# Kernel optimization log

Measured on AMD Instinct MI355X. Metric: run time of the kernel, lower is better.

Reference implementation:

```python
import jax, jax.numpy as jnp
import numpy as np

B, S, DIM, H = 2, 4096, 512, 8
HD = DIM // H
SCALE = HD ** -0.5
EPS = 1e-5


def setup_inputs() -> dict:
    key = jax.random.key(0)
    ks = jax.random.split(key, 7)
    std = DIM ** -0.5
    return {
        "x": jax.random.normal(ks[0], (B, S, DIM), dtype=jnp.float32),
        "ln_gamma": jnp.ones((DIM,), jnp.float32),
        "ln_beta": jnp.zeros((DIM,), jnp.float32),
        "w_q": jax.random.normal(ks[1], (DIM, DIM), jnp.float32) * std,
        "w_k": jax.random.normal(ks[2], (DIM, DIM), jnp.float32) * std,
        "w_v": jax.random.normal(ks[3], (DIM, DIM), jnp.float32) * std,
        "w_fc": jax.random.normal(ks[4], (DIM, DIM), jnp.float32) * std,
    }


def reference(x, ln_gamma, ln_beta, w_q, w_k, w_v, w_fc):
    # LayerNorm over last dim
    mu = jnp.mean(x, axis=-1, keepdims=True)
    var = jnp.var(x, axis=-1, keepdims=True)
    xn = (x - mu) * jax.lax.rsqrt(var + EPS) * ln_gamma + ln_beta
    # QKV projections (torch Linear: y = x @ W.T), split into heads -> [B,H,S,HD]
    q = jnp.einsum('bsd,ed->bse', xn, w_q).reshape(B, S, H, HD).transpose(0, 2, 1, 3)
    k = jnp.einsum('bsd,ed->bse', xn, w_k).reshape(B, S, H, HD).transpose(0, 2, 1, 3)
    v = jnp.einsum('bsd,ed->bse', xn, w_v).reshape(B, S, H, HD).transpose(0, 2, 1, 3)
    # scores [B,H,S,S]
    attn = jnp.einsum('bhqd,bhkd->bhqk', q, k) * SCALE
    attn = jax.nn.softmax(attn, axis=-1)
    # dropout is identity in eval mode
    out = jnp.einsum('bhqk,bhkd->bhqd', attn, v)
    out = out.transpose(0, 2, 1, 3).reshape(B, S, DIM)
    return jnp.einsum('bsd,ed->bse', out, w_fc)
```

## Files before the change

kernel.cpp:

```cpp
#include <hip/hip_runtime.h>
#include <cstdint>
#include <cstddef>

typedef unsigned short u16;
typedef unsigned int   u32;
typedef __bf16 bf16x8 __attribute__((ext_vector_type(8)));
typedef float  f32x4  __attribute__((ext_vector_type(4)));
typedef float  f32x16 __attribute__((ext_vector_type(16)));
typedef u16    u16x8  __attribute__((ext_vector_type(8)));
typedef u16    u16x4  __attribute__((ext_vector_type(4)));
typedef u32    u32x2  __attribute__((ext_vector_type(2)));
typedef u32    u32x4  __attribute__((ext_vector_type(4)));

#define DI __device__ __forceinline__

constexpr int SEQ = 4096;
constexpr int DIM = 512;
constexpr int NH  = 8;
constexpr int HD  = 64;
constexpr float ATT_C1 = 0.125f * 1.44269504088896340736f;

DI u16 f2bf(float f) {
  u32 u = __builtin_bit_cast(u32, f);
  u += 0x7fffu + ((u >> 16) & 1u);
  return (u16)(u >> 16);
}

DI u32 pk2(float hi, float lo) {
  u32 uh = __builtin_bit_cast(u32, hi) + 0x8000u;
  u32 ul = __builtin_bit_cast(u32, lo) + 0x8000u;
  return __builtin_amdgcn_perm(uh, ul, 0x07060302u);
}

DI u32 cvtpk(float a, float b) {
  u32 r;
  asm("v_cvt_pk_bf16_f32 %0, %1, %2" : "=v"(r) : "v"(a), "v"(b));
  return r;
}

DI void plswap(u32& a, u32& b) {
  asm("v_permlane32_swap_b32 %0, %1" : "+v"(a), "+v"(b));
}

__global__ __launch_bounds__(256) void wconv_kernel(
    const float* __restrict__ wq, const float* __restrict__ wk,
    const float* __restrict__ wv, const float* __restrict__ wfc,
    u16* __restrict__ Wb)
{
  const int idx  = blockIdx.x * 256 + threadIdx.x;
  const int base = idx * 8;
  const int mat  = base >> 18;
  const int off  = base & (512 * 512 - 1);
  const float* src = (mat == 0) ? wq : (mat == 1) ? wk : (mat == 2) ? wv : wfc;
  const float4 a = *(const float4*)(src + off);
  const float4 b = *(const float4*)(src + off + 4);
  u32x4 o = { pk2(a.y, a.x), pk2(a.w, a.z), pk2(b.y, b.x), pk2(b.w, b.z) };
  *(u32x4*)(Wb + base) = o;
}

__global__ __launch_bounds__(256) void ln_cast_kernel(
    const float* __restrict__ x, const float* __restrict__ gamma,
    const float* __restrict__ beta, u16* __restrict__ xn)
{
  const int row  = blockIdx.x * 4 + (threadIdx.x >> 6);
  const int lane = threadIdx.x & 63;
  const float* xr = x + (size_t)row * DIM + lane * 8;
  const float4 a = *(const float4*)xr;
  const float4 b = *(const float4*)(xr + 4);
  float s = a.x + a.y + a.z + a.w + b.x + b.y + b.z + b.w;
  float q = a.x*a.x + a.y*a.y + a.z*a.z + a.w*a.w
          + b.x*b.x + b.y*b.y + b.z*b.z + b.w*b.w;
#pragma unroll
  for (int m = 1; m < 64; m <<= 1) {
    s += __shfl_xor(s, m, 64);
    q += __shfl_xor(q, m, 64);
  }
  const float mu = s * (1.0f / DIM);
  const float rs = rsqrtf(q * (1.0f / DIM) - mu * mu + 1e-5f);
  const float4 g0 = *(const float4*)(gamma + lane * 8);
  const float4 g1 = *(const float4*)(gamma + lane * 8 + 4);
  const float4 e0 = *(const float4*)(beta + lane * 8);
  const float4 e1 = *(const float4*)(beta + lane * 8 + 4);
  const float v0 = (a.x - mu) * rs * g0.x + e0.x;
  const float v1 = (a.y - mu) * rs * g0.y + e0.y;
  const float v2 = (a.z - mu) * rs * g0.z + e0.z;
  const float v3 = (a.w - mu) * rs * g0.w + e0.w;
  const float v4 = (b.x - mu) * rs * g1.x + e1.x;
  const float v5 = (b.y - mu) * rs * g1.y + e1.y;
  const float v6 = (b.z - mu) * rs * g1.z + e1.z;
  const float v7 = (b.w - mu) * rs * g1.w + e1.w;
  u32x4 o = { pk2(v1, v0), pk2(v3, v2), pk2(v5, v4), pk2(v7, v6) };
  *(u32x4*)(xn + (size_t)row * DIM + lane * 8) = o;
}

template<int MODE>
__global__ __launch_bounds__(256, 2) void gemm_kernel(
    const u16* __restrict__ A, const u16* __restrict__ Wb,
    u16* __restrict__ Qo, u16* __restrict__ Ko, u16* __restrict__ Vt,
    float* __restrict__ Co)
{
  __shared__ u16 As[128][72];
  __shared__ u16 Bs[128][72];
  const int m0 = blockIdx.y * 128, n0 = blockIdx.x * 128;
  const int t = threadIdx.x, wave = t >> 6, lane = t & 63;
  const int quad = lane >> 4, l15 = lane & 15;
  const int wm = wave >> 1, wn = wave & 1;
  const u16* Wsrc;
  if (MODE == 0) {
    const int mat = n0 >> 9;
    Wsrc = Wb + (size_t)mat * 512 * 512 + (size_t)(n0 & 511) * DIM;
  } else {
    Wsrc = Wb + (size_t)3 * 512 * 512 + (size_t)n0 * DIM;
  }

  f32x4 acc[4][4];
#pragma unroll
  for (int i = 0; i < 4; i++)
#pragma unroll
    for (int j = 0; j < 4; j++)
#pragma unroll
      for (int r = 0; r < 4; r++) acc[i][j][r] = 0.0f;

  for (int kk = 0; kk < DIM; kk += 64) {
    __syncthreads();
#pragma unroll
    for (int it = 0; it < 4; it++) {
      const int c4 = t + it * 256;
      const int r = c4 >> 3, off = (c4 & 7) * 8;
      *(u16x8*)&As[r][off] =
          *(const u16x8*)(A + (size_t)(m0 + r) * DIM + kk + off);
      *(u16x8*)&Bs[r][off] =
          *(const u16x8*)(Wsrc + (size_t)r * DIM + kk + off);
    }
    __syncthreads();
#pragma unroll
    for (int kx = 0; kx < 2; kx++) {
      bf16x8 af[4], bfr[4];
#pragma unroll
      for (int i = 0; i < 4; i++)
        af[i] = *(const bf16x8*)&As[wm * 64 + i * 16 + l15][kx * 32 + quad * 8];
#pragma unroll
      for (int j = 0; j < 4; j++)
        bfr[j] = *(const bf16x8*)&Bs[wn * 64 + j * 16 + l15][kx * 32 + quad * 8];
#pragma unroll
      for (int i = 0; i < 4; i++)
#pragma unroll
        for (int j = 0; j < 4; j++)
          acc[i][j] = __builtin_amdgcn_mfma_f32_16x16x32_bf16(
              af[i], bfr[j], acc[i][j], 0, 0, 0);
    }
  }

  if (MODE == 1) {
#pragma unroll
    for (int i = 0; i < 4; i++) {
      const int m = m0 + wm * 64 + i * 16 + quad * 4;
#pragma unroll
      for (int j = 0; j < 4; j++) {
        const int n = n0 + wn * 64 + j * 16 + l15;
#pragma unroll
        for (int r = 0; r < 4; r++)
          Co[(size_t)(m + r) * DIM + n] = acc[i][j][r];
      }
    }
  } else {
    const int mat = n0 >> 9;
    const float qs = (mat == 0) ? ATT_C1 : 1.0f;
#pragma unroll
    for (int i = 0; i < 4; i++) {
      const int m = m0 + wm * 64 + i * 16 + quad * 4;
      const int b = m >> 12, s = m & 4095;
#pragma unroll
      for (int j = 0; j < 4; j++) {
        const int ng = (n0 & 511) + wn * 64 + j * 16 + l15;
        const int h = ng >> 6, d = ng & 63;
        if (mat < 2) {
          u16* dst = (mat == 0 ? Qo : Ko) +
                     ((size_t)(b * NH + h) * SEQ) * HD + d;
#pragma unroll
          for (int r = 0; r < 4; r++)
            dst[(size_t)(s + r) * HD] = f2bf(acc[i][j][r] * qs);
        } else {
          u32x2 w;
          w[0] = pk2(acc[i][j][1], acc[i][j][0]);
          w[1] = pk2(acc[i][j][3], acc[i][j][2]);
          *(u32x2*)&Vt[((size_t)(b * NH + h) * HD + d) * SEQ + s] = w;
        }
      }
    }
  }
}

__global__ __launch_bounds__(256, 2) void attn_kernel(
    const u16* __restrict__ Q, const u16* __restrict__ K,
    const u16* __restrict__ Vt, u16* __restrict__ O)
{
  __shared__ __align__(16) char smem[36864];
  const int flat = blockIdx.x + 32 * blockIdx.y;
  const int slot = flat >> 3;
  const int bh = (flat & 7) * 2 + (slot & 1);
  const int qt = slot >> 1;
  const int b = bh >> 3, h = bh & 7;
  const int t = threadIdx.x;
  const int wave = t >> 6, lane = t & 63;
  const int kg = wave >> 1;
  const int qsub = wave & 1;
  const int tg = t & 127;
  const int l31 = lane & 31, hf = lane >> 5;

  u16 (*Kl)[72] = (u16 (*)[72])(smem + kg * 18432);
  u16 (*Vl)[72] = (u16 (*)[72])(smem + kg * 18432 + 9216);

  const u16* Qb = Q + (size_t)bh * SEQ * HD;
  const u16* Kb = K + (size_t)bh * SEQ * HD;
  const u16* Vb = Vt + (size_t)bh * HD * SEQ;
  const int qw = qt * 128 + qsub * 64;
  const int kc0 = kg * 2048;

  bf16x8 bq[2][4];
#pragma unroll
  for (int qh = 0; qh < 2; qh++)
#pragma unroll
    for (int kk = 0; kk < 4; kk++)
      bq[qh][kk] = *(const bf16x8*)(
          Qb + (size_t)(qw + qh * 32 + l31) * HD + kk * 16 + hf * 8);

  f32x16 oacc[2][2];
#pragma unroll
  for (int qh = 0; qh < 2; qh++)
#pragma unroll
    for (int mt2 = 0; mt2 < 2; mt2++)
#pragma unroll
      for (int r = 0; r < 16; r++) oacc[qh][mt2][r] = 0.0f;
  float lrun0 = 0.0f, lrun1 = 0.0f;

  u16x8 kst[4], vst[4];
#pragma unroll
  for (int it = 0; it < 4; it++) {
    const int c4 = tg + it * 128;
    const int r = c4 >> 3, off = (c4 & 7) * 8;
    kst[it] = *(const u16x8*)(Kb + (size_t)(kc0 + r) * HD + off);
    vst[it] = *(const u16x8*)(Vb + (size_t)r * SEQ + kc0 + off);
  }

  for (int it2 = 0; it2 < 32; it2++) {
    const int kc = kc0 + it2 * 64;
    __syncthreads();
#pragma unroll
    for (int it = 0; it < 4; it++) {
      const int c4 = tg + it * 128;
      const int r = c4 >> 3, off = (c4 & 7) * 8;
      *(u16x8*)&Kl[r][off] = kst[it];
      *(u16x8*)&Vl[r][off] = vst[it];
    }
    __syncthreads();
    if (it2 < 31) {
#pragma unroll
      for (int it = 0; it < 4; it++) {
        const int c4 = tg + it * 128;
        const int r = c4 >> 3, off = (c4 & 7) * 8;
        kst[it] = *(const u16x8*)(Kb + (size_t)(kc + 64 + r) * HD + off);
        vst[it] = *(const u16x8*)(Vb + (size_t)r * SEQ + kc + 64 + off);
      }
    }

#pragma unroll
    for (int mt = 0; mt < 2; mt++) {
      f32x16 s0, s1;
#pragma unroll
      for (int r = 0; r < 16; r++) { s0[r] = 0.0f; s1[r] = 0.0f; }
      __builtin_amdgcn_s_setprio(1);
#pragma unroll
      for (int kk = 0; kk < 4; kk++) {
        const bf16x8 ka =
            *(const bf16x8*)&Kl[mt * 32 + l31][kk * 16 + hf * 8];
        s0 = __builtin_amdgcn_mfma_f32_32x32x16_bf16(ka, bq[0][kk], s0, 0, 0, 0);
        s1 = __builtin_amdgcn_mfma_f32_32x32x16_bf16(ka, bq[1][kk], s1, 0, 0, 0);
      }
      __builtin_amdgcn_s_setprio(0);

#pragma unroll
      for (int r = 0; r < 16; r++) s0[r] = __builtin_amdgcn_exp2f(s0[r]);
      lrun0 += (((s0[0] + s0[1]) + (s0[2] + s0[3])) +
                ((s0[4] + s0[5]) + (s0[6] + s0[7]))) +
               (((s0[8] + s0[9]) + (s0[10] + s0[11])) +
                ((s0[12] + s0[13]) + (s0[14] + s0[15])));
#pragma unroll
      for (int r = 0; r < 16; r++) s1[r] = __builtin_amdgcn_exp2f(s1[r]);
      lrun1 += (((s1[0] + s1[1]) + (s1[2] + s1[3])) +
                ((s1[4] + s1[5]) + (s1[6] + s1[7]))) +
               (((s1[8] + s1[9]) + (s1[10] + s1[11])) +
                ((s1[12] + s1[13]) + (s1[14] + s1[15])));

      u32 a0 = cvtpk(s0[0],  s0[1]),  a1 = cvtpk(s0[2],  s0[3]);
      u32 a2 = cvtpk(s0[4],  s0[5]),  a3 = cvtpk(s0[6],  s0[7]);
      plswap(a0, a2); plswap(a1, a3);
      u32 c0 = cvtpk(s0[8],  s0[9]),  c1 = cvtpk(s0[10], s0[11]);
      u32 c2 = cvtpk(s0[12], s0[13]), c3 = cvtpk(s0[14], s0[15]);
      plswap(c0, c2); plswap(c1, c3);
      u32x4 p00v = { a0, a1, a2, a3 };
      u32x4 p01v = { c0, c1, c2, c3 };
      u32 d0 = cvtpk(s1[0],  s1[1]),  d1 = cvtpk(s1[2],  s1[3]);
      u32 d2 = cvtpk(s1[4],  s1[5]),  d3 = cvtpk(s1[6],  s1[7]);
      plswap(d0, d2); plswap(d1, d3);
      u32 e0 = cvtpk(s1[8],  s1[9]),  e1 = cvtpk(s1[10], s1[11]);
      u32 e2 = cvtpk(s1[12], s1[13]), e3 = cvtpk(s1[14], s1[15]);
      plswap(e0, e2); plswap(e1, e3);
      u32x4 p10v = { d0, d1, d2, d3 };
      u32x4 p11v = { e0, e1, e2, e3 };
      const bf16x8 p00 = __builtin_bit_cast(bf16x8, p00v);
      const bf16x8 p01 = __builtin_bit_cast(bf16x8, p01v);
      const bf16x8 p10 = __builtin_bit_cast(bf16x8, p10v);
      const bf16x8 p11 = __builtin_bit_cast(bf16x8, p11v);

      __builtin_amdgcn_s_setprio(1);
#pragma unroll
      for (int mt2 = 0; mt2 < 2; mt2++) {
        const bf16x8 va0 =
            *(const bf16x8*)&Vl[mt2 * 32 + l31][(mt * 2 + 0) * 16 + hf * 8];
        oacc[0][mt2] = __builtin_amdgcn_mfma_f32_32x32x16_bf16(
            va0, p00, oacc[0][mt2], 0, 0, 0);
        oacc[1][mt2] = __builtin_amdgcn_mfma_f32_32x32x16_bf16(
            va0, p10, oacc[1][mt2], 0, 0, 0);
        const bf16x8 va1 =
            *(const bf16x8*)&Vl[mt2 * 32 + l31][(mt * 2 + 1) * 16 + hf * 8];
        oacc[0][mt2] = __builtin_amdgcn_mfma_f32_32x32x16_bf16(
            va1, p01, oacc[0][mt2], 0, 0, 0);
        oacc[1][mt2] = __builtin_amdgcn_mfma_f32_32x32x16_bf16(
            va1, p11, oacc[1][mt2], 0, 0, 0);
      }
      __builtin_amdgcn_s_setprio(0);
    }
  }

  __syncthreads();
  f32x4 (*Rbuf)[2][8][64] = (f32x4 (*)[2][8][64])smem;
  float (*Lbuf)[2][64]    = (float (*)[2][64])(smem + 32768);
  if (kg == 1) {
#pragma unroll
    for (int qh = 0; qh < 2; qh++) {
#pragma unroll
      for (int mt2 = 0; mt2 < 2; mt2++)
#pragma unroll
        for (int gi = 0; gi < 4; gi++) {
          f32x4 w;
#pragma unroll
          for (int r = 0; r < 4; r++) w[r] = oacc[qh][mt2][gi * 4 + r];
          Rbuf[qsub][qh][mt2 * 4 + gi][lane] = w;
        }
      Lbuf[qsub][qh][lane] = (qh == 0) ? lrun0 : lrun1;
    }
  }
  __syncthreads();
  if (kg == 0) {
#pragma unroll
    for (int qh = 0; qh < 2; qh++) {
#pragma unroll
      for (int mt2 = 0; mt2 < 2; mt2++)
#pragma unroll
        for (int gi = 0; gi < 4; gi++) {
          const f32x4 w = Rbuf[qsub][qh][mt2 * 4 + gi][lane];
#pragma unroll
          for (int r = 0; r < 4; r++) oacc[qh][mt2][gi * 4 + r] += w[r];
        }
      float lr = ((qh == 0) ? lrun0 : lrun1) + Lbuf[qsub][qh][lane];
      const float lt = lr + __shfl_xor(lr, 32, 64);
      const float inv = 1.0f / lt;
      const int s = qw + qh * 32 + l31;
      u16* Ob = O + ((size_t)(b * SEQ + s)) * DIM + h * HD;
#pragma unroll
      for (int mt2 = 0; mt2 < 2; mt2++)
#pragma unroll
        for (int g = 0; g < 4; g++) {
          u32x2 w;
          w[0] = pk2(oacc[qh][mt2][g * 4 + 1] * inv,
                     oacc[qh][mt2][g * 4 + 0] * inv);
          w[1] = pk2(oacc[qh][mt2][g * 4 + 3] * inv,
                     oacc[qh][mt2][g * 4 + 2] * inv);
          *(u32x2*)&Ob[mt2 * 32 + g * 8 + hf * 4] = w;
        }
    }
  }
}

extern "C" void kernel_launch(void* const* d_in, const int* in_sizes, int n_in,
                              void* d_out, int out_size, void* d_ws,
                              size_t ws_size, hipStream_t stream)
{
  const float* x     = (const float*)d_in[0];
  const float* gamma = (const float*)d_in[1];
  const float* beta  = (const float*)d_in[2];
  const float* wq    = (const float*)d_in[3];
  const float* wk    = (const float*)d_in[4];
  const float* wv    = (const float*)d_in[5];
  const float* wfc   = (const float*)d_in[6];
  float* out = (float*)d_out;

  char* ws = (char*)d_ws;
  u16* xn = (u16*)(ws);
  u16* Qb = (u16*)(ws + ((size_t)8  << 20));
  u16* Kb = (u16*)(ws + ((size_t)16 << 20));
  u16* Vt = (u16*)(ws + ((size_t)24 << 20));
  u16* Ob = (u16*)(ws + ((size_t)32 << 20));
  u16* Wb = (u16*)(ws + ((size_t)40 << 20));

  wconv_kernel<<<512, 256, 0, stream>>>(wq, wk, wv, wfc, Wb);
  ln_cast_kernel<<<2048, 256, 0, stream>>>(x, gamma, beta, xn);
  gemm_kernel<0><<<dim3(12, 64), 256, 0, stream>>>(xn, Wb, Qb, Kb, Vt, nullptr);
  attn_kernel<<<dim3(32, 16), 256, 0, stream>>>(Qb, Kb, Vt, Ob);
  gemm_kernel<1><<<dim3(4, 64), 256, 0, stream>>>(
      Ob, Wb, nullptr, nullptr, nullptr, out);
}
```

Before: 196.7 us.

## Double-buffer attention K/V LDS tiles and use direct global-to-LDS loads in GEMM

The attention loop now keeps two K/V LDS buffers per key group. The next tile is written into the alternate buffer after compute, so each iteration needs one barrier instead of two. The GEMM staging switches to global_load_lds direct copies into unpadded LDS tiles, which skips the register round trip. In exchange, attention LDS use doubles to 72KB, which may cut occupancy, and the unpadded GEMM layout may add LDS bank conflicts on fragment reads.

```diff
diff --git a/kernel.cpp b/kernel.cpp
--- a/kernel.cpp
+++ b/kernel.cpp
@@ -40,6 +40,12 @@
 
 DI void plswap(u32& a, u32& b) {
   asm("v_permlane32_swap_b32 %0, %1" : "+v"(a), "+v"(b));
+}
+
+DI void gl_lds16(const void* g, void* lds) {
+  __builtin_amdgcn_global_load_lds(
+      (const __attribute__((address_space(1))) void*)g,
+      (__attribute__((address_space(3))) void*)lds, 16, 0, 0);
 }
 
 __global__ __launch_bounds__(256) void wconv_kernel(
@@ -99,8 +105,8 @@
     u16* __restrict__ Qo, u16* __restrict__ Ko, u16* __restrict__ Vt,
     float* __restrict__ Co)
 {
-  __shared__ u16 As[128][72];
-  __shared__ u16 Bs[128][72];
+  __shared__ __align__(16) u16 As[128 * 64];
+  __shared__ __align__(16) u16 Bs[128 * 64];
   const int m0 = blockIdx.y * 128, n0 = blockIdx.x * 128;
   const int t = threadIdx.x, wave = t >> 6, lane = t & 63;
   const int quad = lane >> 4, l15 = lane & 15;
@@ -124,13 +130,12 @@
   for (int kk = 0; kk < DIM; kk += 64) {
     __syncthreads();
 #pragma unroll
-    for (int it = 0; it < 4; it++) {
-      const int c4 = t + it * 256;
-      const int r = c4 >> 3, off = (c4 & 7) * 8;
-      *(u16x8*)&As[r][off] =
-          *(const u16x8*)(A + (size_t)(m0 + r) * DIM + kk + off);
-      *(u16x8*)&Bs[r][off] =
-          *(const u16x8*)(Wsrc + (size_t)r * DIM + kk + off);
+    for (int rnd = 0; rnd < 4; rnd++) {
+      const int c4 = t + rnd * 256;
+      const int r = c4 >> 3, cc = (c4 & 7) * 8;
+      const int lbase = (wave + rnd * 4) * 1024;
+      gl_lds16(A + (size_t)(m0 + r) * DIM + kk + cc, (char*)As + lbase);
+      gl_lds16(Wsrc + (size_t)r * DIM + kk + cc, (char*)Bs + lbase);
     }
     __syncthreads();
 #pragma unroll
@@ -138,10 +143,12 @@
       bf16x8 af[4], bfr[4];
 #pragma unroll
       for (int i = 0; i < 4; i++)
-        af[i] = *(const bf16x8*)&As[wm * 64 + i * 16 + l15][kx * 32 + quad * 8];
+        af[i] = *(const bf16x8*)&As[(wm * 64 + i * 16 + l15) * 64 +
+                                    kx * 32 + quad * 8];
 #pragma unroll
       for (int j = 0; j < 4; j++)
-        bfr[j] = *(const bf16x8*)&Bs[wn * 64 + j * 16 + l15][kx * 32 + quad * 8];
+        bfr[j] = *(const bf16x8*)&Bs[(wn * 64 + j * 16 + l15) * 64 +
+                                     kx * 32 + quad * 8];
 #pragma unroll
       for (int i = 0; i < 4; i++)
 #pragma unroll
@@ -195,7 +202,7 @@
     const u16* __restrict__ Q, const u16* __restrict__ K,
     const u16* __restrict__ Vt, u16* __restrict__ O)
 {
-  __shared__ __align__(16) char smem[36864];
+  __shared__ __align__(16) char smem[73728];
   const int flat = blockIdx.x + 32 * blockIdx.y;
   const int slot = flat >> 3;
   const int bh = (flat & 7) * 2 + (slot & 1);
@@ -208,9 +215,6 @@
   const int tg = t & 127;
   const int l31 = lane & 31, hf = lane >> 5;
 
-  u16 (*Kl)[72] = (u16 (*)[72])(smem + kg * 18432);
-  u16 (*Vl)[72] = (u16 (*)[72])(smem + kg * 18432 + 9216);
-
   const u16* Qb = Q + (size_t)bh * SEQ * HD;
   const u16* Kb = K + (size_t)bh * SEQ * HD;
   const u16* Vb = Vt + (size_t)bh * HD * SEQ;
@@ -242,27 +246,30 @@
     kst[it] = *(const u16x8*)(Kb + (size_t)(kc0 + r) * HD + off);
     vst[it] = *(const u16x8*)(Vb + (size_t)r * SEQ + kc0 + off);
   }
-
-  for (int it2 = 0; it2 < 32; it2++) {
-    const int kc = kc0 + it2 * 64;
-    __syncthreads();
+  {
+    u16 (*K0)[72] = (u16 (*)[72])(smem + kg * 36864);
+    u16 (*V0)[72] = (u16 (*)[72])(smem + kg * 36864 + 9216);
 #pragma unroll
     for (int it = 0; it < 4; it++) {
       const int c4 = tg + it * 128;
       const int r = c4 >> 3, off = (c4 & 7) * 8;
-      *(u16x8*)&Kl[r][off] = kst[it];
-      *(u16x8*)&Vl[r][off] = vst[it];
-    }
-    __syncthreads();
-    if (it2 < 31) {
-#pragma unroll
-      for (int it = 0; it < 4; it++) {
-        const int c4 = tg + it * 128;
-        const int r = c4 >> 3, off = (c4 & 7) * 8;
-        kst[it] = *(const u16x8*)(Kb + (size_t)(kc + 64 + r) * HD + off);
-        vst[it] = *(const u16x8*)(Vb + (size_t)r * SEQ + kc + 64 + off);
-      }
-    }
+      *(u16x8*)&K0[r][off] = kst[it];
+      *(u16x8*)&V0[r][off] = vst[it];
+    }
+  }
+#pragma unroll
+  for (int it = 0; it < 4; it++) {
+    const int c4 = tg + it * 128;
+    const int r = c4 >> 3, off = (c4 & 7) * 8;
+    kst[it] = *(const u16x8*)(Kb + (size_t)(kc0 + 64 + r) * HD + off);
+    vst[it] = *(const u16x8*)(Vb + (size_t)r * SEQ + kc0 + 64 + off);
+  }
+  __syncthreads();
+
+  for (int it2 = 0; it2 < 32; it2++) {
+    const int buf = it2 & 1;
+    u16 (*Kl)[72] = (u16 (*)[72])(smem + kg * 36864 + buf * 18432);
+    u16 (*Vl)[72] = (u16 (*)[72])(smem + kg * 36864 + buf * 18432 + 9216);
 
 #pragma unroll
     for (int mt = 0; mt < 2; mt++) {
@@ -331,9 +338,31 @@
       }
       __builtin_amdgcn_s_setprio(0);
     }
-  }
-
-  __syncthreads();
+
+    if (it2 < 31) {
+      u16 (*Kn)[72] = (u16 (*)[72])(smem + kg * 36864 + (buf ^ 1) * 18432);
+      u16 (*Vn)[72] = (u16 (*)[72])(smem + kg * 36864 + (buf ^ 1) * 18432 + 9216);
+#pragma unroll
+      for (int it = 0; it < 4; it++) {
+        const int c4 = tg + it * 128;
+        const int r = c4 >> 3, off = (c4 & 7) * 8;
+        *(u16x8*)&Kn[r][off] = kst[it];
+        *(u16x8*)&Vn[r][off] = vst[it];
+      }
+      if (it2 < 30) {
+        const int kc2 = kc0 + (it2 + 2) * 64;
+#pragma unroll
+        for (int it = 0; it < 4; it++) {
+          const int c4 = tg + it * 128;
+          const int r = c4 >> 3, off = (c4 & 7) * 8;
+          kst[it] = *(const u16x8*)(Kb + (size_t)(kc2 + r) * HD + off);
+          vst[it] = *(const u16x8*)(Vb + (size_t)r * SEQ + kc2 + off);
+        }
+      }
+    }
+    __syncthreads();
+  }
+
   f32x4 (*Rbuf)[2][8][64] = (f32x4 (*)[2][8][64])smem;
   float (*Lbuf)[2][64]    = (float (*)[2][64])(smem + 32768);
   if (kg == 1) {
```

Measured after the change: 198.3 us. Within noise of the previous version (+0.8%).
